# Performance work log

Hardware: AMD Instinct MI355X
Metric: run time of the kernel (lower is better)

The kernel has to match this reference:

```python
import jax, jax.numpy as jnp
import numpy as np

B, L, D = 8, 2048, 64
EPS = 1e-8


def setup_inputs() -> dict:
    key = jax.random.key(0)
    ks = jax.random.split(key, 7)
    s = 1.0 / np.sqrt(D)  # ~ torch Linear default init scale
    return {
        "x": jax.random.normal(ks[0], (B, L, D), dtype=jnp.float32),
        "B_w": jax.random.normal(ks[1], (D, D), dtype=jnp.float32) * s,
        "B_b": jax.random.normal(ks[2], (D,), dtype=jnp.float32) * s,
        "C_w": jax.random.normal(ks[3], (D, D), dtype=jnp.float32) * s,
        "C_b": jax.random.normal(ks[4], (D,), dtype=jnp.float32) * s,
        "V_w": jax.random.normal(ks[5], (D, D), dtype=jnp.float32) * s,
        "V_b": jax.random.normal(ks[6], (D,), dtype=jnp.float32) * s,
    }


def reference(x, B_w, B_b, C_w, C_b, V_w, V_b):
    # torch nn.Linear: y = x @ W.T + b
    BZ = jnp.einsum('bld,ed->ble', x, B_w) + B_b   # (B,L,D)
    CZ = jnp.einsum('bld,ed->ble', x, C_w) + C_b   # (B,L,D)
    scores = jnp.einsum('bld,bmd->blm', BZ, CZ)     # (B,L,L)
    attn = jax.nn.relu(scores)
    # note: normalization over dim=-2 (column sums), as in the original
    attn = attn / (attn.sum(axis=-2, keepdims=True) + EPS)
    VZ = jnp.einsum('bld,ed->ble', x, V_w) + V_b   # (B,L,D)
    out = jnp.einsum('blm,bmd->bld', attn, VZ)      # (B,L,D)
    return x + out
```

## Files before the change

kernel.cpp:

```cpp
#include <hip/hip_runtime.h>

typedef unsigned short u16;
typedef unsigned int u32;
typedef __bf16 bf16x8 __attribute__((ext_vector_type(8)));
typedef float f32x16 __attribute__((ext_vector_type(16)));
typedef const void __attribute__((address_space(1))) gvoid;
typedef void __attribute__((address_space(3))) lvoid;

#define GLOAD16(gp, lp) __builtin_amdgcn_global_load_lds((gvoid*)(gp), (lvoid*)(lp), 16, 0, 0)

namespace {
constexpr int Ln = 2048;
constexpr float EPS = 1e-8f;
}

__device__ __forceinline__ u16 f2bf(float f) {
  __bf16 h = (__bf16)f;
  return __builtin_bit_cast(u16, h);
}

__global__ __launch_bounds__(512) void proj_k(
    const float* __restrict__ x,
    const float* __restrict__ Bw, const float* __restrict__ Bb,
    const float* __restrict__ Cw, const float* __restrict__ Cb,
    const float* __restrict__ Vw, const float* __restrict__ Vb,
    u16* __restrict__ BZh, u16* __restrict__ CZh, u16* __restrict__ VZTh)
{
    __shared__ float xs[64][65];
    __shared__ float Bt[64][65];
    __shared__ float Ct[64][65];
    __shared__ float Vt[64][65];
    __shared__ float vt[64][68];
    const int tid = threadIdx.x;
    const int r0 = (int)blockIdx.x * 64;
    for (int i = 0; i < 8; ++i) {
        int f = i * 512 + tid;
        int e = f >> 6, d = f & 63;
        Bt[d][e] = Bw[f];
        Ct[d][e] = Cw[f];
        Vt[d][e] = Vw[f];
        xs[e][d] = x[r0 * 64 + f];
    }
    __syncthreads();
    const int e  = tid & 63;
    const int lbase = (tid >> 6) * 8;
    const float bb = Bb[e], cb = Cb[e], vb = Vb[e];
    float aB[8], aC[8], aV[8];
    #pragma unroll
    for (int j = 0; j < 8; ++j) { aB[j] = bb; aC[j] = cb; aV[j] = vb; }
    for (int d = 0; d < 64; ++d) {
        const float wB = Bt[d][e], wC = Ct[d][e], wV = Vt[d][e];
        #pragma unroll
        for (int j = 0; j < 8; ++j) {
            const float xv = xs[lbase + j][d];
            aB[j] += xv * wB; aC[j] += xv * wC; aV[j] += xv * wV;
        }
    }
    #pragma unroll
    for (int j = 0; j < 8; ++j) {
        const int g = (r0 + lbase + j) * 64 + e;
        BZh[g] = f2bf(aB[j]);
        CZh[g] = f2bf(aC[j]);
        vt[e][lbase + j] = aV[j];
    }
    __syncthreads();
    const int d  = tid >> 3;
    const int lc = (tid & 7) * 8;
    const int bq  = r0 >> 11;
    const int l0b = r0 & 2047;
    u16 pk8[8];
    #pragma unroll
    for (int t = 0; t < 8; ++t) pk8[t] = f2bf(vt[d][lc + t]);
    uint4 pv;
    pv.x = (u32)pk8[0] | ((u32)pk8[1] << 16);
    pv.y = (u32)pk8[2] | ((u32)pk8[3] << 16);
    pv.z = (u32)pk8[4] | ((u32)pk8[5] << 16);
    pv.w = (u32)pk8[6] | ((u32)pk8[7] << 16);
    *(uint4*)(VZTh + ((bq * 64 + d) * Ln + l0b + lc)) = pv;
}

__global__ __launch_bounds__(512) void denom_k(
    const u16* __restrict__ BZh, const u16* __restrict__ CZh,
    float* __restrict__ colsum)
{
    __shared__ __attribute__((aligned(16))) char smem2[16384 + 64 * 4 * 4];
    char* const BZs2 = smem2;
    float* const red = (float*)(smem2 + 16384);
    const int tid = threadIdx.x;
    const int lane = tid & 63;
    const int ln = lane & 31;
    const int g5 = lane >> 5;
    const int w  = tid >> 6;
    const int wm2 = w & 1, wl2 = w >> 1;
    const int b  = blockIdx.y;
    const int mb = blockIdx.x * 64;
    const int wave_base = tid & ~63;

    bf16x8 af[4];
    {
        const int m = mb + wm2 * 32 + ln;
        const u16* cp = CZh + ((b * Ln + m) << 6) + g5 * 8;
        #pragma unroll
        for (int c = 0; c < 4; ++c) af[c] = *(const bf16x8*)(cp + c * 16);
    }
    float accs[16];
    #pragma unroll
    for (int r = 0; r < 16; ++r) accs[r] = 0.f;
    const int lrr = wl2 * 32 + ln;
    for (int lt0 = 0; lt0 < Ln; lt0 += 128) {
        __syncthreads();
        #pragma unroll
        for (int it = 0; it < 2; ++it) {
            int j = (it << 9) + tid;
            int r = j >> 3;
            int u = (j & 7) ^ (r & 7);
            const u16* src = BZh + ((b * Ln + lt0 + r) << 6) + (u << 3);
            GLOAD16(src, BZs2 + ((it << 9) + wave_base) * 16);
        }
        __syncthreads();
        f32x16 st = {};
        #pragma unroll
        for (int c = 0; c < 4; ++c) {
            int un = (c << 1) | g5;
            bf16x8 bfr = *(const bf16x8*)(BZs2 + (lrr << 7) + ((un ^ (lrr & 7)) << 4));
            st = __builtin_amdgcn_mfma_f32_32x32x16_bf16(af[c], bfr, st, 0, 0, 0);
        }
        #pragma unroll
        for (int r = 0; r < 16; ++r) accs[r] += fmaxf(st[r], 0.f);
    }
    #pragma unroll
    for (int msk = 1; msk <= 16; msk <<= 1)
        #pragma unroll
        for (int r = 0; r < 16; ++r)
            accs[r] += __shfl_xor(accs[r], msk, 64);
    if (ln == 0) {
        #pragma unroll
        for (int r = 0; r < 16; ++r) {
            int mloc = wm2 * 32 + (r & 3) + ((r >> 2) << 3) + g5 * 4;
            red[mloc * 4 + wl2] = accs[r];
        }
    }
    __syncthreads();
    if (tid < 64)
        colsum[b * Ln + mb + tid] = red[tid*4+0] + red[tid*4+1] + red[tid*4+2] + red[tid*4+3];
}

__global__ __launch_bounds__(512) void fused_out(
    const float* __restrict__ x,
    const u16* __restrict__ BZh, const u16* __restrict__ CZh,
    const u16* __restrict__ VZTh, const float* __restrict__ colsum,
    float* __restrict__ out)
{
    __shared__ __attribute__((aligned(16))) char smem[98304];
    char* const BZs = smem;
    char* const Pb  = smem + 8192;
    float* const denl = (float*)(smem + 24576);
    const int tid = threadIdx.x;
    const int lane = tid & 63;
    const int ln = lane & 31;
    const int g5 = lane >> 5;
    const int w  = tid >> 6;
    const int b  = blockIdx.y;
    const int l0 = blockIdx.x * 64;
    const int wave_base = tid & ~63;

    auto stage = [&](int m0s, int bi) {
        char* bufc = smem + 32768 + (bi << 15);
        char* vzb  = bufc + 16384;
        #pragma unroll
        for (int it = 0; it < 2; ++it) {
            int j = (it << 9) + tid;
            int r = j >> 3;
            int u = (j & 7) ^ (r & 7);
            const u16* src = CZh + ((b * Ln + m0s + r) << 6) + (u << 3);
            GLOAD16(src, bufc + ((it << 9) + wave_base) * 16);
        }
        #pragma unroll
        for (int it = 0; it < 2; ++it) {
            int j = (it << 9) + tid;
            int r = j >> 4;
            int u = (j & 15) ^ (r & 7);
            const u16* src = VZTh + ((b << 6) + r) * Ln + m0s + (u << 3);
            GLOAD16(src, vzb + ((it << 9) + wave_base) * 16);
        }
    };

    {
        int j = tid;
        int r = j >> 3;
        int u = (j & 7) ^ (r & 7);
        const u16* src = BZh + ((b * Ln + l0 + r) << 6) + (u << 3);
        GLOAD16(src, BZs + (wave_base << 4));
    }
    {
        const float4 cs = *(const float4*)(colsum + b * Ln + tid * 4);
        float4 dv;
        dv.x = 1.f / (cs.x + EPS); dv.y = 1.f / (cs.y + EPS);
        dv.z = 1.f / (cs.z + EPS); dv.w = 1.f / (cs.w + EPS);
        *(float4*)(denl + tid * 4) = dv;
    }
    stage(0, 0);
    __syncthreads();

    f32x16 acc = {};
    const int wm = w & 3, wl = w >> 2;
    const int wt = w >> 1, ws2 = w & 1;
    const int dt = wt >> 1, lt = wt & 1;
    const int mrA = wm * 32 + ln;
    const int lrA = wl * 32 + ln;
    const int drB = dt * 32 + ln;
    const int lrB = lt * 32 + ln;

    for (int cI = 0; cI < 16; ++cI) {
        const int cur = cI & 1;
        if (cI < 15) stage((cI + 1) << 7, cur ^ 1);
        const char* cz = smem + 32768 + (cur << 15);
        f32x16 st = {};
        #pragma unroll
        for (int c = 0; c < 4; ++c) {
            int un = (c << 1) | g5;
            bf16x8 a   = *(const bf16x8*)(cz  + (mrA << 7) + ((un ^ (mrA & 7)) << 4));
            bf16x8 bfr = *(const bf16x8*)(BZs + (lrA << 7) + ((un ^ (lrA & 7)) << 4));
            st = __builtin_amdgcn_mfma_f32_32x32x16_bf16(a, bfr, st, 0, 0, 0);
        }
        const int mbase = (cI << 7) + wm * 32;
        #pragma unroll
        for (int q = 0; q < 4; ++q) {
            const int mq = mbase + q * 8 + g5 * 4;
            float p0 = fmaxf(st[q*4+0], 0.f) * denl[mq + 0];
            float p1 = fmaxf(st[q*4+1], 0.f) * denl[mq + 1];
            float p2 = fmaxf(st[q*4+2], 0.f) * denl[mq + 2];
            float p3 = fmaxf(st[q*4+3], 0.f) * denl[mq + 3];
            uint2 pk;
            pk.x = (u32)f2bf(p0) | ((u32)f2bf(p1) << 16);
            pk.y = (u32)f2bf(p2) | ((u32)f2bf(p3) << 16);
            *(uint2*)(Pb + (lrA << 8) + ((((wm << 2) | q) ^ (lrA & 7)) << 4) + (g5 << 3)) = pk;
        }
        asm volatile("s_waitcnt lgkmcnt(0)" ::: "memory");
        __builtin_amdgcn_s_barrier();
        asm volatile("" ::: "memory");
        const char* vz = cz + 16384;
        #pragma unroll
        for (int c = 0; c < 4; ++c) {
            int un = (ws2 << 3) | (c << 1) | g5;
            bf16x8 av = *(const bf16x8*)(vz + (drB << 8) + ((un ^ (drB & 7)) << 4));
            bf16x8 bp = *(const bf16x8*)(Pb + (lrB << 8) + ((un ^ (lrB & 7)) << 4));
            acc = __builtin_amdgcn_mfma_f32_32x32x16_bf16(av, bp, acc, 0, 0, 0);
        }
        asm volatile("s_waitcnt vmcnt(0) lgkmcnt(0)" ::: "memory");
        __builtin_amdgcn_s_barrier();
        asm volatile("" ::: "memory");
    }

    __syncthreads();
    float* redf = (float*)(smem + 32768);
    if (ws2 == 1) {
        #pragma unroll
        for (int r = 0; r < 16; ++r) redf[(wt * 64 + lane) * 17 + r] = acc[r];
    }
    __syncthreads();
    if (ws2 == 0) {
        #pragma unroll
        for (int r = 0; r < 16; ++r) acc[r] += redf[(wt * 64 + lane) * 17 + r];
        const int row = b * Ln + l0 + lt * 32 + ln;
        #pragma unroll
        for (int q = 0; q < 4; ++q) {
            const int d = dt * 32 + q * 8 + g5 * 4;
            const float4 xv = *(const float4*)(x + row * 64 + d);
            float4 o;
            o.x = xv.x + acc[q*4+0];
            o.y = xv.y + acc[q*4+1];
            o.z = xv.z + acc[q*4+2];
            o.w = xv.w + acc[q*4+3];
            *(float4*)(out + row * 64 + d) = o;
        }
    }
}

extern "C" void kernel_launch(void* const* d_in, const int* in_sizes, int n_in,
                              void* d_out, int out_size, void* d_ws, size_t ws_size,
                              hipStream_t stream) {
    const float* x  = (const float*)d_in[0];
    const float* Bw = (const float*)d_in[1];
    const float* Bb = (const float*)d_in[2];
    const float* Cw = (const float*)d_in[3];
    const float* Cb = (const float*)d_in[4];
    const float* Vw = (const float*)d_in[5];
    const float* Vb = (const float*)d_in[6];
    float* out = (float*)d_out;
    char* wsb = (char*)d_ws;
    u16* BZh  = (u16*)wsb;
    u16* CZh  = (u16*)(wsb + (2u << 20));
    u16* VZTh = (u16*)(wsb + (4u << 20));
    float* colsum = (float*)(wsb + (6u << 20));

    proj_k<<<dim3(256), 512, 0, stream>>>(x, Bw, Bb, Cw, Cb, Vw, Vb, BZh, CZh, VZTh);
    denom_k<<<dim3(32, 8), 512, 0, stream>>>(BZh, CZh, colsum);
    fused_out<<<dim3(32, 8), 512, 0, stream>>>(x, BZh, CZh, VZTh, colsum, out);
}
```

Measured before the change: 56.30 us.

## Triple-buffer loads, split denom over L halves, keep P in registers

The denominator kernel is split across two halves of L via a third grid dimension, which doubles its block count, and it now uses a triple-buffered async load pipeline with partial vmcnt waits. The output kernel also moves to triple buffering with a single barrier per iteration. It keeps the BZ fragments in registers and builds the P operand through cross-lane half swaps instead of an LDS round trip. Each wave now owns all 64 D columns over its own m slice, so a three-step LDS reduction and a coalesced epilogue are added. In exchange it uses more LDS and registers, which may lower occupancy, and the fragment-swap layout is easy to get wrong.

```diff
diff --git a/kernel.cpp b/kernel.cpp
--- a/kernel.cpp
+++ b/kernel.cpp
@@ -8,6 +8,7 @@
 typedef void __attribute__((address_space(3))) lvoid;
 
 #define GLOAD16(gp, lp) __builtin_amdgcn_global_load_lds((gvoid*)(gp), (lvoid*)(lp), 16, 0, 0)
+#define POST_BARRIER_FENCE() do { __builtin_amdgcn_sched_barrier(0); asm volatile("" ::: "memory"); } while (0)
 
 namespace {
 constexpr int Ln = 2048;
@@ -17,6 +18,20 @@
 __device__ __forceinline__ u16 f2bf(float f) {
   __bf16 h = (__bf16)f;
   return __builtin_bit_cast(u16, h);
+}
+
+__device__ __forceinline__ u32 pk2(float lo, float hi) {
+    u32 r;
+    asm("v_cvt_pk_bf16_f32 %0, %1, %2" : "=v"(r) : "v"(lo), "v"(hi));
+    return r;
+}
+
+__device__ __forceinline__ void half_swap(u32 a, u32 b, u32& na, u32& nb) {
+    u32 sa = (u32)__shfl_xor((int)a, 32, 64);
+    u32 sb = (u32)__shfl_xor((int)b, 32, 64);
+    int hi = (threadIdx.x & 63) >> 5;
+    na = hi ? a : sb;
+    nb = hi ? sa : b;
 }
 
 __global__ __launch_bounds__(512) void proj_k(
@@ -81,50 +96,63 @@
 
 __global__ __launch_bounds__(512) void denom_k(
     const u16* __restrict__ BZh, const u16* __restrict__ CZh,
-    float* __restrict__ colsum)
+    float* __restrict__ denp)
 {
-    __shared__ __attribute__((aligned(16))) char smem2[16384 + 64 * 4 * 4];
-    char* const BZs2 = smem2;
-    float* const red = (float*)(smem2 + 16384);
+    __shared__ __attribute__((aligned(16))) char smem2[49152 + 1024];
+    float* const red = (float*)(smem2 + 49152);
     const int tid = threadIdx.x;
     const int lane = tid & 63;
     const int ln = lane & 31;
     const int g5 = lane >> 5;
-    const int w  = tid >> 6;
+    const int w = tid >> 6;
     const int wm2 = w & 1, wl2 = w >> 1;
-    const int b  = blockIdx.y;
+    const int b = blockIdx.y;
     const int mb = blockIdx.x * 64;
+    const int half = blockIdx.z;
+    const int l0h = half * 1024;
     const int wave_base = tid & ~63;
 
     bf16x8 af[4];
     {
-        const int m = mb + wm2 * 32 + ln;
-        const u16* cp = CZh + ((b * Ln + m) << 6) + g5 * 8;
+        const u16* cp = CZh + ((b * Ln + mb + wm2 * 32 + ln) << 6) + g5 * 8;
         #pragma unroll
         for (int c = 0; c < 4; ++c) af[c] = *(const bf16x8*)(cp + c * 16);
     }
-    float accs[16];
-    #pragma unroll
-    for (int r = 0; r < 16; ++r) accs[r] = 0.f;
-    const int lrr = wl2 * 32 + ln;
-    for (int lt0 = 0; lt0 < Ln; lt0 += 128) {
-        __syncthreads();
+    auto stageD = [&](int t) {
+        char* buf = smem2 + (t % 3) * 16384;
         #pragma unroll
         for (int it = 0; it < 2; ++it) {
             int j = (it << 9) + tid;
             int r = j >> 3;
             int u = (j & 7) ^ (r & 7);
-            const u16* src = BZh + ((b * Ln + lt0 + r) << 6) + (u << 3);
-            GLOAD16(src, BZs2 + ((it << 9) + wave_base) * 16);
-        }
-        __syncthreads();
+            GLOAD16(BZh + ((b * Ln + l0h + t * 128 + r) << 6) + (u << 3),
+                    buf + ((it << 9) + wave_base) * 16);
+        }
+    };
+    stageD(0); stageD(1);
+    __syncthreads();
+    float accs[16];
+    #pragma unroll
+    for (int r = 0; r < 16; ++r) accs[r] = 0.f;
+    const int lr = wl2 * 32 + ln;
+    for (int t = 0; t < 8; ++t) {
+        if (t > 0) {
+            if (t < 7) asm volatile("s_waitcnt vmcnt(2)" ::: "memory");
+            else       asm volatile("s_waitcnt vmcnt(0)" ::: "memory");
+            __builtin_amdgcn_s_barrier();
+            POST_BARRIER_FENCE();
+        }
+        if (t + 2 < 8) stageD(t + 2);
+        const char* buf = smem2 + (t % 3) * 16384;
         f32x16 st = {};
+        __builtin_amdgcn_s_setprio(1);
         #pragma unroll
         for (int c = 0; c < 4; ++c) {
             int un = (c << 1) | g5;
-            bf16x8 bfr = *(const bf16x8*)(BZs2 + (lrr << 7) + ((un ^ (lrr & 7)) << 4));
+            bf16x8 bfr = *(const bf16x8*)(buf + (lr << 7) + ((un ^ (lr & 7)) << 4));
             st = __builtin_amdgcn_mfma_f32_32x32x16_bf16(af[c], bfr, st, 0, 0, 0);
         }
+        __builtin_amdgcn_s_setprio(0);
         #pragma unroll
         for (int r = 0; r < 16; ++r) accs[r] += fmaxf(st[r], 0.f);
     }
@@ -142,138 +170,190 @@
     }
     __syncthreads();
     if (tid < 64)
-        colsum[b * Ln + mb + tid] = red[tid*4+0] + red[tid*4+1] + red[tid*4+2] + red[tid*4+3];
+        denp[(half * 8 + b) * Ln + mb + tid] =
+            red[tid*4+0] + red[tid*4+1] + red[tid*4+2] + red[tid*4+3];
 }
 
 __global__ __launch_bounds__(512) void fused_out(
     const float* __restrict__ x,
     const u16* __restrict__ BZh, const u16* __restrict__ CZh,
-    const u16* __restrict__ VZTh, const float* __restrict__ colsum,
+    const u16* __restrict__ VZTh, const float* __restrict__ denp,
     float* __restrict__ out)
 {
-    __shared__ __attribute__((aligned(16))) char smem[98304];
+    __shared__ __attribute__((aligned(16))) char smem[114688];
     char* const BZs = smem;
-    char* const Pb  = smem + 8192;
-    float* const denl = (float*)(smem + 24576);
+    float* const denl = (float*)(smem + 8192);
+    char* const bufs = smem + 16384;
     const int tid = threadIdx.x;
     const int lane = tid & 63;
     const int ln = lane & 31;
     const int g5 = lane >> 5;
-    const int w  = tid >> 6;
-    const int b  = blockIdx.y;
+    const int w = tid >> 6;
+    const int wm = w & 3;
+    const int wl = w >> 2;
+    const int b = blockIdx.y;
     const int l0 = blockIdx.x * 64;
     const int wave_base = tid & ~63;
 
-    auto stage = [&](int m0s, int bi) {
-        char* bufc = smem + 32768 + (bi << 15);
-        char* vzb  = bufc + 16384;
+    auto stage = [&](int t) {
+        char* bufc = bufs + (t % 3) * 32768;
+        char* vzb = bufc + 16384;
+        const int m0s = t << 7;
         #pragma unroll
         for (int it = 0; it < 2; ++it) {
             int j = (it << 9) + tid;
             int r = j >> 3;
             int u = (j & 7) ^ (r & 7);
-            const u16* src = CZh + ((b * Ln + m0s + r) << 6) + (u << 3);
-            GLOAD16(src, bufc + ((it << 9) + wave_base) * 16);
+            GLOAD16(CZh + ((b * Ln + m0s + r) << 6) + (u << 3),
+                    bufc + ((it << 9) + wave_base) * 16);
         }
         #pragma unroll
         for (int it = 0; it < 2; ++it) {
             int j = (it << 9) + tid;
             int r = j >> 4;
             int u = (j & 15) ^ (r & 7);
-            const u16* src = VZTh + ((b << 6) + r) * Ln + m0s + (u << 3);
-            GLOAD16(src, vzb + ((it << 9) + wave_base) * 16);
+            GLOAD16(VZTh + ((b << 6) + r) * Ln + m0s + (u << 3),
+                    vzb + ((it << 9) + wave_base) * 16);
         }
     };
 
     {
-        int j = tid;
-        int r = j >> 3;
-        int u = (j & 7) ^ (r & 7);
-        const u16* src = BZh + ((b * Ln + l0 + r) << 6) + (u << 3);
-        GLOAD16(src, BZs + (wave_base << 4));
-    }
-    {
-        const float4 cs = *(const float4*)(colsum + b * Ln + tid * 4);
+        int r = tid >> 3;
+        int u = (tid & 7) ^ (r & 7);
+        GLOAD16(BZh + ((b * Ln + l0 + r) << 6) + (u << 3), BZs + wave_base * 16);
+    }
+    {
+        const float4 c0 = *(const float4*)(denp + b * Ln + tid * 4);
+        const float4 c1 = *(const float4*)(denp + (8 + b) * Ln + tid * 4);
         float4 dv;
-        dv.x = 1.f / (cs.x + EPS); dv.y = 1.f / (cs.y + EPS);
-        dv.z = 1.f / (cs.z + EPS); dv.w = 1.f / (cs.w + EPS);
+        dv.x = 1.f / (c0.x + c1.x + EPS);
+        dv.y = 1.f / (c0.y + c1.y + EPS);
+        dv.z = 1.f / (c0.z + c1.z + EPS);
+        dv.w = 1.f / (c0.w + c1.w + EPS);
         *(float4*)(denl + tid * 4) = dv;
     }
-    stage(0, 0);
-    __syncthreads();
-
-    f32x16 acc = {};
-    const int wm = w & 3, wl = w >> 2;
-    const int wt = w >> 1, ws2 = w & 1;
-    const int dt = wt >> 1, lt = wt & 1;
-    const int mrA = wm * 32 + ln;
-    const int lrA = wl * 32 + ln;
-    const int drB = dt * 32 + ln;
-    const int lrB = lt * 32 + ln;
-
-    for (int cI = 0; cI < 16; ++cI) {
-        const int cur = cI & 1;
-        if (cI < 15) stage((cI + 1) << 7, cur ^ 1);
-        const char* cz = smem + 32768 + (cur << 15);
-        f32x16 st = {};
+    stage(0); stage(1);
+    __syncthreads();
+
+    bf16x8 bzf[4];
+    {
+        const int lr = wl * 32 + ln;
         #pragma unroll
         for (int c = 0; c < 4; ++c) {
             int un = (c << 1) | g5;
-            bf16x8 a   = *(const bf16x8*)(cz  + (mrA << 7) + ((un ^ (mrA & 7)) << 4));
-            bf16x8 bfr = *(const bf16x8*)(BZs + (lrA << 7) + ((un ^ (lrA & 7)) << 4));
-            st = __builtin_amdgcn_mfma_f32_32x32x16_bf16(a, bfr, st, 0, 0, 0);
-        }
-        const int mbase = (cI << 7) + wm * 32;
+            bzf[c] = *(const bf16x8*)(BZs + (lr << 7) + ((un ^ (lr & 7)) << 4));
+        }
+    }
+    f32x16 acc0 = {}, acc1 = {};
+    const int mA = wm * 32 + ln;
+
+    for (int t = 0; t < 16; ++t) {
+        if (t > 0) {
+            if (t < 15) asm volatile("s_waitcnt vmcnt(4)" ::: "memory");
+            else        asm volatile("s_waitcnt vmcnt(0)" ::: "memory");
+            __builtin_amdgcn_s_barrier();
+            POST_BARRIER_FENCE();
+        }
+        if (t + 2 < 16) stage(t + 2);
+        const char* cz = bufs + (t % 3) * 32768;
+        const char* vz = cz + 16384;
+        f32x16 st = {};
+        __builtin_amdgcn_s_setprio(1);
+        #pragma unroll
+        for (int c = 0; c < 4; ++c) {
+            int un = (c << 1) | g5;
+            bf16x8 a = *(const bf16x8*)(cz + (mA << 7) + ((un ^ (mA & 7)) << 4));
+            st = __builtin_amdgcn_mfma_f32_32x32x16_bf16(a, bzf[c], st, 0, 0, 0);
+        }
+        __builtin_amdgcn_s_setprio(0);
+        const int mq0 = (t << 7) + wm * 32;
+        u32 wv[8];
         #pragma unroll
         for (int q = 0; q < 4; ++q) {
-            const int mq = mbase + q * 8 + g5 * 4;
-            float p0 = fmaxf(st[q*4+0], 0.f) * denl[mq + 0];
-            float p1 = fmaxf(st[q*4+1], 0.f) * denl[mq + 1];
-            float p2 = fmaxf(st[q*4+2], 0.f) * denl[mq + 2];
-            float p3 = fmaxf(st[q*4+3], 0.f) * denl[mq + 3];
-            uint2 pk;
-            pk.x = (u32)f2bf(p0) | ((u32)f2bf(p1) << 16);
-            pk.y = (u32)f2bf(p2) | ((u32)f2bf(p3) << 16);
-            *(uint2*)(Pb + (lrA << 8) + ((((wm << 2) | q) ^ (lrA & 7)) << 4) + (g5 << 3)) = pk;
-        }
-        asm volatile("s_waitcnt lgkmcnt(0)" ::: "memory");
-        __builtin_amdgcn_s_barrier();
-        asm volatile("" ::: "memory");
-        const char* vz = cz + 16384;
-        #pragma unroll
-        for (int c = 0; c < 4; ++c) {
-            int un = (ws2 << 3) | (c << 1) | g5;
-            bf16x8 av = *(const bf16x8*)(vz + (drB << 8) + ((un ^ (drB & 7)) << 4));
-            bf16x8 bp = *(const bf16x8*)(Pb + (lrB << 8) + ((un ^ (lrB & 7)) << 4));
-            acc = __builtin_amdgcn_mfma_f32_32x32x16_bf16(av, bp, acc, 0, 0, 0);
-        }
-        asm volatile("s_waitcnt vmcnt(0) lgkmcnt(0)" ::: "memory");
-        __builtin_amdgcn_s_barrier();
-        asm volatile("" ::: "memory");
-    }
-
-    __syncthreads();
-    float* redf = (float*)(smem + 32768);
-    if (ws2 == 1) {
-        #pragma unroll
-        for (int r = 0; r < 16; ++r) redf[(wt * 64 + lane) * 17 + r] = acc[r];
-    }
-    __syncthreads();
-    if (ws2 == 0) {
-        #pragma unroll
-        for (int r = 0; r < 16; ++r) acc[r] += redf[(wt * 64 + lane) * 17 + r];
-        const int row = b * Ln + l0 + lt * 32 + ln;
+            const float4 dq = *(const float4*)(denl + mq0 + q * 8 + g5 * 4);
+            float p0 = fmaxf(st[q*4+0], 0.f) * dq.x;
+            float p1 = fmaxf(st[q*4+1], 0.f) * dq.y;
+            float p2 = fmaxf(st[q*4+2], 0.f) * dq.z;
+            float p3 = fmaxf(st[q*4+3], 0.f) * dq.w;
+            wv[q*2+0] = pk2(p0, p1);
+            wv[q*2+1] = pk2(p2, p3);
+        }
+        u32 f0w0, f0w1, f0w2, f0w3, f1w0, f1w1, f1w2, f1w3;
+        half_swap(wv[2], wv[0], f0w2, f0w0);
+        half_swap(wv[3], wv[1], f0w3, f0w1);
+        half_swap(wv[6], wv[4], f1w2, f1w0);
+        half_swap(wv[7], wv[5], f1w3, f1w1);
+        bf16x8 pf0, pf1;
+        { uint4 t4; t4.x=f0w0; t4.y=f0w1; t4.z=f0w2; t4.w=f0w3; pf0 = __builtin_bit_cast(bf16x8, t4); }
+        { uint4 t4; t4.x=f1w0; t4.y=f1w1; t4.z=f1w2; t4.w=f1w3; pf1 = __builtin_bit_cast(bf16x8, t4); }
+        const int un00 = (wm << 2) | g5;
+        const int un01 = (wm << 2) | 2 | g5;
+        __builtin_amdgcn_s_setprio(1);
+        {
+            bf16x8 av;
+            av = *(const bf16x8*)(vz + (ln << 8) + ((un00 ^ (ln & 7)) << 4));
+            acc0 = __builtin_amdgcn_mfma_f32_32x32x16_bf16(av, pf0, acc0, 0, 0, 0);
+            av = *(const bf16x8*)(vz + (ln << 8) + ((un01 ^ (ln & 7)) << 4));
+            acc0 = __builtin_amdgcn_mfma_f32_32x32x16_bf16(av, pf1, acc0, 0, 0, 0);
+            av = *(const bf16x8*)(vz + ((32 + ln) << 8) + ((un00 ^ (ln & 7)) << 4));
+            acc1 = __builtin_amdgcn_mfma_f32_32x32x16_bf16(av, pf0, acc1, 0, 0, 0);
+            av = *(const bf16x8*)(vz + ((32 + ln) << 8) + ((un01 ^ (ln & 7)) << 4));
+            acc1 = __builtin_amdgcn_mfma_f32_32x32x16_bf16(av, pf1, acc1, 0, 0, 0);
+        }
+        __builtin_amdgcn_s_setprio(0);
+    }
+
+    __syncthreads();
+    float* red = (float*)(bufs);
+    constexpr int LSTR = 36;
+    constexpr int SSTR = 64 * LSTR;
+    if (wm >= 2) {
+        float* base = red + (wl * 2 + (wm - 2)) * SSTR + lane * LSTR;
+        #pragma unroll
+        for (int r = 0; r < 16; ++r) { base[r] = acc0[r]; base[16 + r] = acc1[r]; }
+    }
+    __syncthreads();
+    if (wm < 2) {
+        float* base = red + (wl * 2 + wm) * SSTR + lane * LSTR;
+        #pragma unroll
+        for (int r = 0; r < 16; ++r) { acc0[r] += base[r]; acc1[r] += base[16 + r]; }
+    }
+    if (wm == 1) {
+        float* base = red + (4 + wl) * SSTR + lane * LSTR;
+        #pragma unroll
+        for (int r = 0; r < 16; ++r) { base[r] = acc0[r]; base[16 + r] = acc1[r]; }
+    }
+    __syncthreads();
+    float* lout = (float*)(smem + 81920);
+    if (wm == 0) {
+        float* base = red + (4 + wl) * SSTR + lane * LSTR;
+        #pragma unroll
+        for (int r = 0; r < 16; ++r) { acc0[r] += base[r]; acc1[r] += base[16 + r]; }
+        const int lrow = wl * 32 + ln;
         #pragma unroll
         for (int q = 0; q < 4; ++q) {
-            const int d = dt * 32 + q * 8 + g5 * 4;
-            const float4 xv = *(const float4*)(x + row * 64 + d);
-            float4 o;
-            o.x = xv.x + acc[q*4+0];
-            o.y = xv.y + acc[q*4+1];
-            o.z = xv.z + acc[q*4+2];
-            o.w = xv.w + acc[q*4+3];
-            *(float4*)(out + row * 64 + d) = o;
-        }
+            const int d0 = q * 8 + g5 * 4;
+            float4 v0;
+            v0.x = acc0[q*4+0]; v0.y = acc0[q*4+1]; v0.z = acc0[q*4+2]; v0.w = acc0[q*4+3];
+            *(float4*)(lout + lrow * 68 + d0) = v0;
+            float4 v1;
+            v1.x = acc1[q*4+0]; v1.y = acc1[q*4+1]; v1.z = acc1[q*4+2]; v1.w = acc1[q*4+3];
+            *(float4*)(lout + lrow * 68 + 32 + d0) = v1;
+        }
+    }
+    __syncthreads();
+    {
+        const int row = tid >> 3;
+        const int dc = (tid & 7) * 8;
+        const int g = (b * Ln + l0 + row) * 64 + dc;
+        float4 o0 = *(const float4*)(lout + row * 68 + dc);
+        float4 o1 = *(const float4*)(lout + row * 68 + dc + 4);
+        const float4 x0 = *(const float4*)(x + g);
+        const float4 x1 = *(const float4*)(x + g + 4);
+        o0.x += x0.x; o0.y += x0.y; o0.z += x0.z; o0.w += x0.w;
+        o1.x += x1.x; o1.y += x1.y; o1.z += x1.z; o1.w += x1.w;
+        *(float4*)(out + g) = o0;
+        *(float4*)(out + g + 4) = o1;
     }
 }
 
@@ -292,9 +372,9 @@
     u16* BZh  = (u16*)wsb;
     u16* CZh  = (u16*)(wsb + (2u << 20));
     u16* VZTh = (u16*)(wsb + (4u << 20));
-    float* colsum = (float*)(wsb + (6u << 20));
+    float* denp = (float*)(wsb + (6u << 20));
 
     proj_k<<<dim3(256), 512, 0, stream>>>(x, Bw, Bb, Cw, Cb, Vw, Vb, BZh, CZh, VZTh);
-    denom_k<<<dim3(32, 8), 512, 0, stream>>>(BZh, CZh, colsum);
-    fused_out<<<dim3(32, 8), 512, 0, stream>>>(x, BZh, CZh, VZTh, colsum, out);
-}
+    denom_k<<<dim3(32, 8, 2), 512, 0, stream>>>(BZh, CZh, denp);
+    fused_out<<<dim3(32, 8), 512, 0, stream>>>(x, BZh, CZh, VZTh, denp, out);
+}
```

Measured after the change: 53.81 us. -4.4%, faster.
